# Performance work log

Hardware: AMD Instinct MI355X
Metric: run time of the kernel (lower is better)

The kernel has to match this reference:

```python
import jax, jax.numpy as jnp
import numpy as np

B, S, D = 4, 2048, 1024
H = 16
HD = D // H

def setup_inputs() -> dict:
    key = jax.random.key(0)
    ks = jax.random.split(key, 6)
    std = 1.0 / np.sqrt(D)
    x = jax.random.normal(ks[0], (B, S, D), dtype=jnp.float32)
    Wq = jax.random.uniform(ks[1], (D, D), jnp.float32, -std, std)
    Wk = jax.random.uniform(ks[2], (D, D), jnp.float32, -std, std)
    Wv = jax.random.uniform(ks[3], (D, D), jnp.float32, -std, std)
    Wo = jax.random.uniform(ks[4], (D, D), jnp.float32, -std, std)
    bo = jax.random.uniform(ks[5], (D,), jnp.float32, -std, std)
    return {"x": x, "Wq": Wq, "Wk": Wk, "Wv": Wv, "Wo": Wo, "bo": bo}

def reference(x, Wq, Wk, Wv, Wo, bo):
    b, s, _ = x.shape
    # projections; torch Linear computes x @ W^T, here W stored as (d_in, d_out)... we use (D, D) applied as x @ W
    q = (x @ Wq).reshape(b, s, H, HD).transpose(0, 2, 1, 3)  # b h s hd
    k = (x @ Wk).reshape(b, s, H, HD).transpose(0, 2, 1, 3)
    v = (x @ Wv).reshape(b, s, H, HD).transpose(0, 2, 1, 3)
    scores = jnp.einsum('bhqd,bhkd->bhqk', q, k)
    causal = jnp.triu(jnp.ones((s, s), dtype=bool), k=1)
    scores = jnp.where(causal[None, None], -jnp.inf, scores)
    attn = jax.nn.softmax(scores / np.sqrt(HD), axis=-1)  # dropout=0.0 -> identity
    ctx = jnp.einsum('bhqk,bhkd->bhqd', attn, v)
    ctx = ctx.transpose(0, 2, 1, 3).reshape(b, s, D)
    return ctx @ Wo + bo
```

## Files before the change

kernel.cpp:

```cpp
#include <hip/hip_runtime.h>

typedef unsigned short u16;
typedef __bf16 bf16x8 __attribute__((ext_vector_type(8)));
typedef float f32x4 __attribute__((ext_vector_type(4)));

#define Bn 4
#define Sn 2048
#define Dn 1024
#define Hn 16
#define HDn 64

__device__ inline u16 f2bf(float f) {
  unsigned u = __builtin_bit_cast(unsigned, f);
  u += 0x7fffu + ((u >> 16) & 1u);
  return (u16)(u >> 16);
}

__device__ __forceinline__ void gl2lds16(const u16* g, u16* l) {
  __builtin_amdgcn_global_load_lds(
      (const __attribute__((address_space(1))) unsigned int*)g,
      (__attribute__((address_space(3))) unsigned int*)l, 16, 0, 0);
}

__device__ __forceinline__ float fexp2(float x) {
  return __builtin_amdgcn_exp2f(x);
}

__device__ __forceinline__ unsigned pk_bf_trunc(float lo, float hi) {
  return __builtin_amdgcn_perm(__builtin_bit_cast(unsigned, hi),
                               __builtin_bit_cast(unsigned, lo), 0x07060302u);
}

__global__ __launch_bounds__(256) void cvt4(const float* __restrict__ in,
                                            u16* __restrict__ out, int n4) {
  int i = blockIdx.x * 256 + threadIdx.x;
  if (i < n4) {
    float4 v = ((const float4*)in)[i];
    ushort4 o;
    o.x = f2bf(v.x); o.y = f2bf(v.y); o.z = f2bf(v.z); o.w = f2bf(v.w);
    ((ushort4*)out)[i] = o;
  }
}

__global__ __launch_bounds__(256) void tcvt4(const float* __restrict__ w0,
                                             const float* __restrict__ w1,
                                             const float* __restrict__ w2,
                                             const float* __restrict__ w3,
                                             u16* __restrict__ out) {
  __shared__ u16 tile[32][33];
  const float* in = (blockIdx.z == 0) ? w0 : (blockIdx.z == 1) ? w1
                   : (blockIdx.z == 2) ? w2 : w3;
  u16* dst = out + (size_t)blockIdx.z * Dn * Dn;
  int bx = blockIdx.x * 32;
  int by = blockIdx.y * 32;
  int tx = threadIdx.x & 31;
  int ty = threadIdx.x >> 5;
#pragma unroll
  for (int r = 0; r < 32; r += 8)
    tile[ty + r][tx] = f2bf(in[(size_t)(by + ty + r) * Dn + bx + tx]);
  __syncthreads();
#pragma unroll
  for (int r = 0; r < 32; r += 8)
    dst[(size_t)(bx + ty + r) * Dn + by + tx] = tile[tx][ty + r];
}

__global__ __launch_bounds__(512, 2) void gemm_qkv(const u16* __restrict__ A,
                                                   const u16* __restrict__ Bt,
                                                   u16* __restrict__ qkb,
                                                   u16* __restrict__ vt,
                                                   float qscale) {
  __shared__ __attribute__((aligned(16))) u16 S[2][4][8192];

  const int tid = threadIdx.x;
  const int lane = tid & 63;
  const int lcol = lane & 15;
  const int quad = lane >> 4;
  const int wave = tid >> 6;
  const int wr = wave >> 2;
  const int wc = wave & 3;

  const int bid = blockIdx.x;
  const int swz = (bid & 7) * 48 + (bid >> 3);
  const int bm = (swz & 31) * 256;
  const int bn = (swz >> 5) * 256;

  const u16* srcp[4][2];
#pragma unroll
  for (int rg = 0; rg < 4; rg++) {
#pragma unroll
    for (int j = 0; j < 2; j++) {
      int o = j * 8192 + tid * 16;
      int l = o ^ (((o >> 8) & 7) << 4);
      int rho = l >> 7;
      int c2 = (l >> 1) & 63;
      int gr;
      if (rg == 0)      gr = bm + (rho & 63) + ((rho >> 6) << 7);
      else if (rg == 1) gr = bm + 64 + (rho & 63) + ((rho >> 6) << 7);
      else if (rg == 2) gr = bn + ((rho >> 5) << 6) + (rho & 31);
      else              gr = bn + ((rho >> 5) << 6) + 32 + (rho & 31);
      const u16* base = (rg < 2) ? A : Bt;
      srcp[rg][j] = base + (size_t)gr * Dn + c2;
    }
  }

  auto stg = [&](int rg, int buf, int tile) {
    if (tile >= 16) return;
    const int k0 = tile << 6;
    u16* d = &S[buf][rg][tid * 8];
    gl2lds16(srcp[rg][0] + k0, d);
    gl2lds16(srcp[rg][1] + k0, d + 4096);
  };

  f32x4 acc[8][4];
#pragma unroll
  for (int i = 0; i < 8; i++)
#pragma unroll
    for (int j = 0; j < 4; j++) acc[i][j] = (f32x4){0.f, 0.f, 0.f, 0.f};

  const int SW = (lcol & 14) << 3;
  const int cs0 = (quad * 16) ^ SW;
  const int cs1 = (64 + quad * 16) ^ SW;

#define PHASE(BUF, QR, QC, STG_STMT, WAIT_STMT)                               \
  {                                                                           \
    const char* Ab = (const char*)&S[BUF][QR][0];                             \
    const char* Bb = (const char*)&S[BUF][2 + QC][0];                         \
    bf16x8 af0[4], af1[4], bf0[2], bf1[2];                                    \
    _Pragma("unroll") for (int mi = 0; mi < 4; mi++) {                        \
      int r = (wr * 64 + mi * 16 + lcol) * 128;                               \
      af0[mi] = *(const bf16x8*)(Ab + (r + cs0));                             \
      af1[mi] = *(const bf16x8*)(Ab + (r + cs1));                             \
    }                                                                         \
    _Pragma("unroll") for (int ni = 0; ni < 2; ni++) {                        \
      int r = (wc * 32 + ni * 16 + lcol) * 128;                               \
      bf0[ni] = *(const bf16x8*)(Bb + (r + cs0));                             \
      bf1[ni] = *(const bf16x8*)(Bb + (r + cs1));                             \
    }                                                                         \
    STG_STMT;                                                                 \
    WAIT_STMT;                                                                \
    __builtin_amdgcn_s_barrier();                                             \
    asm volatile("s_waitcnt lgkmcnt(0)" ::: "memory");                        \
    __builtin_amdgcn_sched_barrier(0);                                        \
    __builtin_amdgcn_s_setprio(1);                                            \
    _Pragma("unroll") for (int mi = 0; mi < 4; mi++)                          \
      _Pragma("unroll") for (int ni = 0; ni < 2; ni++) {                      \
        acc[QR * 4 + mi][QC * 2 + ni] =                                       \
            __builtin_amdgcn_mfma_f32_16x16x32_bf16(                          \
                af0[mi], bf0[ni], acc[QR * 4 + mi][QC * 2 + ni], 0, 0, 0);    \
        acc[QR * 4 + mi][QC * 2 + ni] =                                       \
            __builtin_amdgcn_mfma_f32_16x16x32_bf16(                          \
                af1[mi], bf1[ni], acc[QR * 4 + mi][QC * 2 + ni], 0, 0, 0);    \
      }                                                                       \
    __builtin_amdgcn_s_setprio(0);                                            \
    __builtin_amdgcn_s_barrier();                                             \
  }

  stg(0, 0, 0); stg(2, 0, 0); stg(1, 0, 0); stg(3, 0, 0);
  stg(0, 1, 1); stg(2, 1, 1);
  asm volatile("s_waitcnt vmcnt(4)" ::: "memory");
  __builtin_amdgcn_s_barrier();

#pragma unroll 1
  for (int I = 0; I < 8; ++I) {
    const int t1 = 2 * I + 1, t2 = 2 * I + 2, t3 = 2 * I + 3;
    PHASE(0, 0, 0, stg(1, 1, t1), );
    PHASE(0, 0, 1, stg(3, 1, t1), );
    PHASE(0, 1, 0, stg(0, 0, t2), );
    PHASE(0, 1, 1, stg(2, 0, t2),
          if (I < 7) asm volatile("s_waitcnt vmcnt(4)" ::: "memory");
          else asm volatile("s_waitcnt vmcnt(0)" ::: "memory"));
    PHASE(1, 0, 0, stg(1, 0, t2), );
    PHASE(1, 0, 1, stg(3, 0, t2), );
    PHASE(1, 1, 0, stg(0, 1, t3), );
    PHASE(1, 1, 1, stg(2, 1, t3),
          if (I < 7) asm volatile("s_waitcnt vmcnt(4)" ::: "memory"));
  }
#undef PHASE

  const int rb = bm + wr * 128 + quad * 4;
  const int cb = bn + wc * 64 + lcol;
  if (bn >= 2048) {
#pragma unroll
    for (int ai = 0; ai < 8; ai++) {
#pragma unroll
      for (int bj = 0; bj < 4; bj++) {
        int row0 = rb + ((ai >> 2) << 6) + ((ai & 3) << 4);
        int s = row0 & (Sn - 1);
        int bb = row0 >> 11;
        int vcol = cb + ((bj >> 1) << 5) + ((bj & 1) << 4) - 2048;
        int bh = (bb << 4) + (vcol >> 6);
        int hd = vcol & 63;
        unsigned d0 = (unsigned)f2bf(acc[ai][bj][0]) |
                      ((unsigned)f2bf(acc[ai][bj][1]) << 16);
        unsigned d1 = (unsigned)f2bf(acc[ai][bj][2]) |
                      ((unsigned)f2bf(acc[ai][bj][3]) << 16);
        *(uint2*)(vt + ((size_t)bh * HDn + hd) * Sn + s) = (uint2){d0, d1};
      }
    }
  } else {
    const float scale = (bn < 1024) ? qscale : 1.0f;
#pragma unroll
    for (int ai = 0; ai < 8; ai++) {
#pragma unroll
      for (int bj = 0; bj < 4; bj++) {
        int row0 = rb + ((ai >> 2) << 6) + ((ai & 3) << 4);
        int col = cb + ((bj >> 1) << 5) + ((bj & 1) << 4);
#pragma unroll
        for (int r = 0; r < 4; r++)
          qkb[(size_t)(row0 + r) * 2048 + col] = f2bf(acc[ai][bj][r] * scale);
      }
    }
  }
}

__global__ __launch_bounds__(256) void gemm_out(const u16* __restrict__ A,
                                                const u16* __restrict__ Bt,
                                                float* __restrict__ Cout,
                                                const float* __restrict__ bias) {
  __shared__ __attribute__((aligned(16))) u16 As[2][2][128][32];
  __shared__ __attribute__((aligned(16))) u16 Bs[2][2][128][32];
  const int K = Dn;
  const int t = threadIdx.x;
  const int wave = t >> 6;
  const int lane = t & 63;
  const int lcol = lane & 15;
  const int quad = lane >> 4;
  const int wm = (wave >> 1) * 64;
  const int wn = (wave & 1) * 64;
  const int bm = blockIdx.y * 128;
  const int bn = blockIdx.x * 128;

  const int srow = lane >> 2;
  const int sseg = (lane & 3) * 8;
  const u16* a0p = A + (size_t)(bm + wave * 16 + srow) * K + sseg;
  const u16* a1p = a0p + (size_t)64 * K;
  const u16* b0p = Bt + (size_t)(bn + wave * 16 + srow) * K + sseg;
  const u16* b1p = b0p + (size_t)64 * K;
  u16* asl = &As[0][0][0][0] + wave * 512 + lane * 8;
  u16* bsl = &Bs[0][0][0][0] + wave * 512 + lane * 8;

  auto stage = [&](int k0, int d) {
    u16* as = asl + d * 8192;
    u16* bs = bsl + d * 8192;
    gl2lds16(a0p + k0, as);
    gl2lds16(a1p + k0, as + 2048);
    gl2lds16(a0p + k0 + 32, as + 4096);
    gl2lds16(a1p + k0 + 32, as + 6144);
    gl2lds16(b0p + k0, bs);
    gl2lds16(b1p + k0, bs + 2048);
    gl2lds16(b0p + k0 + 32, bs + 4096);
    gl2lds16(b1p + k0 + 32, bs + 6144);
  };

  f32x4 acc[4][4];
#pragma unroll
  for (int i = 0; i < 4; i++)
#pragma unroll
    for (int j = 0; j < 4; j++) acc[i][j] = (f32x4){0.f, 0.f, 0.f, 0.f};

  stage(0, 0);
  int d = 0;
  for (int k0 = 0; k0 < K; k0 += 64, d ^= 1) {
    __syncthreads();
    if (k0 + 64 < K) stage(k0 + 64, d ^ 1);
#pragma unroll
    for (int ks = 0; ks < 2; ks++) {
      bf16x8 af[4], bf[4];
#pragma unroll
      for (int mi = 0; mi < 4; mi++)
        af[mi] = *(const bf16x8*)(&As[d][ks][wm + mi * 16 + lcol][quad * 8]);
#pragma unroll
      for (int ni = 0; ni < 4; ni++)
        bf[ni] = *(const bf16x8*)(&Bs[d][ks][wn + ni * 16 + lcol][quad * 8]);
#pragma unroll
      for (int mi = 0; mi < 4; mi++)
#pragma unroll
        for (int ni = 0; ni < 4; ni++)
          acc[mi][ni] = __builtin_amdgcn_mfma_f32_16x16x32_bf16(af[mi], bf[ni], acc[mi][ni], 0, 0, 0);
    }
  }

#pragma unroll
  for (int mi = 0; mi < 4; mi++) {
#pragma unroll
    for (int ni = 0; ni < 4; ni++) {
#pragma unroll
      for (int r = 0; r < 4; r++) {
        int row = bm + wm + mi * 16 + quad * 4 + r;
        int col = bn + wn + ni * 16 + lcol;
        Cout[(size_t)row * Dn + col] = acc[mi][ni][r] + bias[col];
      }
    }
  }
}

__global__ __launch_bounds__(256, 2) void attn5(const u16* __restrict__ QK,
                                                const u16* __restrict__ Vt,
                                                u16* __restrict__ ctx) {
  __shared__ __attribute__((aligned(16))) u16 Ks2[2][64][32];
  __shared__ __attribute__((aligned(16))) u16 Vts2[2][64][32];
  __shared__ __attribute__((aligned(16))) u16 Pt[4][32][72];

  const int bh = blockIdx.x;
  const int b = bh >> 4, h = bh & 15;
  const int pair = blockIdx.y;
  const int t = threadIdx.x;
  const int w = t >> 6;
  const int lane = t & 63;
  const int lcol = lane & 15;
  const int quad = lane >> 4;
  const int qw0 = pair * 128 + w * 32;
  const int qw1 = (15 - pair) * 128 + w * 32;

  const size_t qkbase = ((size_t)b * Sn) * 2048 + h * HDn;
  const size_t obase = ((size_t)b * Sn) * Dn + h * HDn;
  const size_t vbase = ((size_t)bh * HDn) * Sn;

  bf16x8 qf[2][2][2];
#pragma unroll
  for (int si = 0; si < 2; si++) {
    const int qws = si ? qw1 : qw0;
#pragma unroll
    for (int qb = 0; qb < 2; qb++) {
      const u16* qp = QK + qkbase + (size_t)(qws + qb * 16 + lcol) * 2048 + quad * 8;
      qf[si][qb][0] = *(const bf16x8*)qp;
      qf[si][qb][1] = *(const bf16x8*)(qp + 32);
    }
  }

  f32x4 o[2][2][4];
#pragma unroll
  for (int si = 0; si < 2; si++)
#pragma unroll
    for (int qb = 0; qb < 2; qb++)
#pragma unroll
      for (int nb = 0; nb < 4; nb++) o[si][qb][nb] = (f32x4){0.f, 0.f, 0.f, 0.f};
  float lsum[2][2] = {{0.f, 0.f}, {0.f, 0.f}};

  const int srow = lane >> 2;
  const int sseg = (lane & 3) * 8;
  const u16* kp0 = QK + qkbase + 1024 + (size_t)(w * 16 + srow) * 2048 + sseg;
  const u16* vp0 = Vt + vbase + (size_t)(w * 16 + srow) * Sn + sseg;
  u16* ksl0 = &Ks2[0][0][0] + w * 512 + lane * 8;
  u16* ksl1 = ksl0 + 2048;
  u16* vsl0 = &Vts2[0][0][0] + w * 512 + lane * 8;
  u16* vsl1 = vsl0 + 2048;

  auto do_strip = [&](int si, int qw, int j0) {
    f32x4 s[4][2];
#pragma unroll
    for (int mb = 0; mb < 4; mb++) {
      bf16x8 kf0 = *(const bf16x8*)(&Ks2[0][mb * 16 + lcol][quad * 8]);
      bf16x8 kf1 = *(const bf16x8*)(&Ks2[1][mb * 16 + lcol][quad * 8]);
#pragma unroll
      for (int qb = 0; qb < 2; qb++) {
        f32x4 a = (f32x4){0.f, 0.f, 0.f, 0.f};
        a = __builtin_amdgcn_mfma_f32_16x16x32_bf16(kf0, qf[si][qb][0], a, 0, 0, 0);
        a = __builtin_amdgcn_mfma_f32_16x16x32_bf16(kf1, qf[si][qb][1], a, 0, 0, 0);
        s[mb][qb] = a;
      }
    }

    const bool needmask = (j0 + 63 > qw);
#pragma unroll
    for (int qb = 0; qb < 2; qb++) {
      const int qrow = qw + qb * 16 + lcol;
#pragma unroll
      for (int mb = 0; mb < 4; mb++) {
        float p[4];
#pragma unroll
        for (int r = 0; r < 4; r++) p[r] = fexp2(s[mb][qb][r]);
        if (needmask) {
          const int kvb = j0 + mb * 16 + quad * 4;
#pragma unroll
          for (int r = 0; r < 4; r++)
            if (kvb + r > qrow) p[r] = 0.f;
        }
        lsum[si][qb] += (p[0] + p[1]) + (p[2] + p[3]);
        unsigned d0 = pk_bf_trunc(p[0], p[1]);
        unsigned d1 = pk_bf_trunc(p[2], p[3]);
        *(uint2*)(&Pt[w][qb * 16 + lcol][mb * 16 + quad * 4]) = (uint2){d0, d1};
      }
    }

#pragma unroll
    for (int c = 0; c < 2; c++) {
      bf16x8 pf0 = *(const bf16x8*)(&Pt[w][lcol][c * 32 + quad * 8]);
      bf16x8 pf1 = *(const bf16x8*)(&Pt[w][16 + lcol][c * 32 + quad * 8]);
#pragma unroll
      for (int nb = 0; nb < 4; nb++) {
        bf16x8 vf = *(const bf16x8*)(&Vts2[c][nb * 16 + lcol][quad * 8]);
        o[si][0][nb] = __builtin_amdgcn_mfma_f32_16x16x32_bf16(vf, pf0, o[si][0][nb], 0, 0, 0);
        o[si][1][nb] = __builtin_amdgcn_mfma_f32_16x16x32_bf16(vf, pf1, o[si][1][nb], 0, 0, 0);
      }
    }
  };

  const int n_kv = (15 - pair) * 128 + 128;

  for (int j0 = 0; j0 < n_kv; j0 += 64) {
    {
      const u16* kp = kp0 + (size_t)j0 * 2048;
      gl2lds16(kp, ksl0);
      gl2lds16(kp + 32, ksl1);
      const u16* vp = vp0 + j0;
      gl2lds16(vp, vsl0);
      gl2lds16(vp + 32, vsl1);
    }
    __syncthreads();

    if (j0 <= qw1 + 31) do_strip(1, qw1, j0);
    if (j0 <= qw0 + 31) do_strip(0, qw0, j0);
    __syncthreads();
  }

#pragma unroll
  for (int si = 0; si < 2; si++) {
    const int qws = si ? qw1 : qw0;
#pragma unroll
    for (int qb = 0; qb < 2; qb++) {
      float l = lsum[si][qb];
      l += __shfl_xor(l, 16);
      l += __shfl_xor(l, 32);
      float inv = 1.0f / l;
#pragma unroll
      for (int nb = 0; nb < 4; nb++) {
        unsigned d0 = (unsigned)f2bf(o[si][qb][nb][0] * inv) |
                      ((unsigned)f2bf(o[si][qb][nb][1] * inv) << 16);
        unsigned d1 = (unsigned)f2bf(o[si][qb][nb][2] * inv) |
                      ((unsigned)f2bf(o[si][qb][nb][3] * inv) << 16);
        u16* p = ctx + obase + (size_t)(qws + qb * 16 + lcol) * Dn + nb * 16 + quad * 4;
        *(uint2*)p = (uint2){d0, d1};
      }
    }
  }
}

extern "C" void kernel_launch(void* const* d_in, const int* in_sizes, int n_in,
                              void* d_out, int out_size, void* d_ws, size_t ws_size,
                              hipStream_t stream) {
  const float* x  = (const float*)d_in[0];
  const float* Wq = (const float*)d_in[1];
  const float* Wk = (const float*)d_in[2];
  const float* Wv = (const float*)d_in[3];
  const float* Wo = (const float*)d_in[4];
  const float* bo = (const float*)d_in[5];
  float* out = (float*)d_out;

  const size_t BSD = (size_t)Bn * Sn * Dn;
  const size_t DD = (size_t)Dn * Dn;

  u16* xb    = (u16*)d_ws;
  u16* wall  = xb + BSD;
  u16* qkb   = wall + 4 * DD;
  u16* vt    = qkb + 2 * BSD;
  u16* cb    = vt + BSD;

  cvt4<<<(int)(BSD / 4 / 256), 256, 0, stream>>>(x, xb, (int)(BSD / 4));
  tcvt4<<<dim3(Dn / 32, Dn / 32, 4), 256, 0, stream>>>(Wq, Wk, Wv, Wo, wall);

  gemm_qkv<<<dim3(384), 512, 0, stream>>>(xb, wall, qkb, vt,
                                          0.125f * 1.44269504f);

  attn5<<<dim3(Bn * Hn, 8), 256, 0, stream>>>(qkb, vt, cb);

  gemm_out<<<dim3(Dn / 128, (Bn * Sn) / 128), 256, 0, stream>>>(cb, wall + 3 * DD, out, bo);
}
```

Baseline: 253.3 us.

## Restructure QKV GEMM main loop to cache B fragments and reorder staging

```diff
diff --git a/kernel.cpp b/kernel.cpp
--- a/kernel.cpp
+++ b/kernel.cpp
@@ -80,9 +80,8 @@
   const int wc = wave & 3;
 
   const int bid = blockIdx.x;
-  const int swz = (bid & 7) * 48 + (bid >> 3);
-  const int bm = (swz & 31) * 256;
-  const int bn = (swz >> 5) * 256;
+  const int bm = ((bid & 7) * 4 + ((bid >> 3) & 3)) * 256;
+  const int bn = (bid >> 5) * 256;
 
   const u16* srcp[4][2];
 #pragma unroll
@@ -121,61 +120,67 @@
   const int cs0 = (quad * 16) ^ SW;
   const int cs1 = (64 + quad * 16) ^ SW;
 
-#define PHASE(BUF, QR, QC, STG_STMT, WAIT_STMT)                               \
-  {                                                                           \
-    const char* Ab = (const char*)&S[BUF][QR][0];                             \
-    const char* Bb = (const char*)&S[BUF][2 + QC][0];                         \
-    bf16x8 af0[4], af1[4], bf0[2], bf1[2];                                    \
-    _Pragma("unroll") for (int mi = 0; mi < 4; mi++) {                        \
-      int r = (wr * 64 + mi * 16 + lcol) * 128;                               \
-      af0[mi] = *(const bf16x8*)(Ab + (r + cs0));                             \
-      af1[mi] = *(const bf16x8*)(Ab + (r + cs1));                             \
-    }                                                                         \
-    _Pragma("unroll") for (int ni = 0; ni < 2; ni++) {                        \
-      int r = (wc * 32 + ni * 16 + lcol) * 128;                               \
-      bf0[ni] = *(const bf16x8*)(Bb + (r + cs0));                             \
-      bf1[ni] = *(const bf16x8*)(Bb + (r + cs1));                             \
-    }                                                                         \
-    STG_STMT;                                                                 \
-    WAIT_STMT;                                                                \
-    __builtin_amdgcn_s_barrier();                                             \
-    asm volatile("s_waitcnt lgkmcnt(0)" ::: "memory");                        \
-    __builtin_amdgcn_sched_barrier(0);                                        \
-    __builtin_amdgcn_s_setprio(1);                                            \
-    _Pragma("unroll") for (int mi = 0; mi < 4; mi++)                          \
-      _Pragma("unroll") for (int ni = 0; ni < 2; ni++) {                      \
-        acc[QR * 4 + mi][QC * 2 + ni] =                                       \
-            __builtin_amdgcn_mfma_f32_16x16x32_bf16(                          \
-                af0[mi], bf0[ni], acc[QR * 4 + mi][QC * 2 + ni], 0, 0, 0);    \
-        acc[QR * 4 + mi][QC * 2 + ni] =                                       \
-            __builtin_amdgcn_mfma_f32_16x16x32_bf16(                          \
-                af1[mi], bf1[ni], acc[QR * 4 + mi][QC * 2 + ni], 0, 0, 0);    \
-      }                                                                       \
-    __builtin_amdgcn_s_setprio(0);                                            \
-    __builtin_amdgcn_s_barrier();                                             \
-  }
-
-  stg(0, 0, 0); stg(2, 0, 0); stg(1, 0, 0); stg(3, 0, 0);
-  stg(0, 1, 1); stg(2, 1, 1);
-  asm volatile("s_waitcnt vmcnt(4)" ::: "memory");
+  bf16x8 bk0[4], bk1[4];
+
+#define MFMA16(a, b, c) __builtin_amdgcn_mfma_f32_16x16x32_bf16(a, b, c, 0, 0, 0)
+
+#define ARD(D, Q, F, K)                                                      \
+  (*(const bf16x8*)((const char*)&S[D][(Q) >> 1][0] +                        \
+      ((wr * 64 + ((Q) & 1) * 32 + (F) * 16 + lcol) * 128 +                  \
+       ((K) ? cs1 : cs0))))
+#define BRD(D, NI, K)                                                        \
+  (*(const bf16x8*)((const char*)&S[D][2 + ((NI) >> 1)][0] +                 \
+      ((wc * 32 + ((NI) & 1) * 16 + lcol) * 128 + ((K) ? cs1 : cs0))))
+
+#define PHASE(D, T, Q, DO_B, STG_RG, WAIT)                                   \
+  {                                                                          \
+    bf16x8 a00 = ARD(D, Q, 0, 0), a01 = ARD(D, Q, 0, 1);                     \
+    bf16x8 a10 = ARD(D, Q, 1, 0), a11 = ARD(D, Q, 1, 1);                     \
+    if (DO_B) {                                                              \
+      _Pragma("unroll") for (int ni = 0; ni < 4; ni++) {                     \
+        bk0[ni] = BRD(D, ni, 0);                                             \
+        bk1[ni] = BRD(D, ni, 1);                                             \
+      }                                                                      \
+    }                                                                        \
+    stg(STG_RG, (D) ^ 1, (T) + 1);                                           \
+    WAIT;                                                                    \
+    __builtin_amdgcn_s_barrier();                                            \
+    asm volatile("s_waitcnt lgkmcnt(0)" ::: "memory");                       \
+    __builtin_amdgcn_sched_barrier(0);                                       \
+    __builtin_amdgcn_s_setprio(1);                                           \
+    _Pragma("unroll") for (int ni = 0; ni < 4; ni++) {                       \
+      acc[(Q) * 2][ni] = MFMA16(a00, bk0[ni], acc[(Q) * 2][ni]);             \
+      acc[(Q) * 2][ni] = MFMA16(a01, bk1[ni], acc[(Q) * 2][ni]);             \
+      acc[(Q) * 2 + 1][ni] = MFMA16(a10, bk0[ni], acc[(Q) * 2 + 1][ni]);     \
+      acc[(Q) * 2 + 1][ni] = MFMA16(a11, bk1[ni], acc[(Q) * 2 + 1][ni]);     \
+    }                                                                        \
+    __builtin_amdgcn_s_setprio(0);                                           \
+    __builtin_amdgcn_s_barrier();                                            \
+  }
+
+#define TILE(D, T)                                                           \
+  PHASE(D, T, 0, 1, 2, )                                                     \
+  PHASE(D, T, 1, 0, 3,                                                       \
+        if ((T) < 15) asm volatile("s_waitcnt vmcnt(4)" ::: "memory");       \
+        else asm volatile("s_waitcnt vmcnt(0)" ::: "memory"))                \
+  PHASE(D, T, 2, 0, 0, )                                                     \
+  PHASE(D, T, 3, 0, 1, asm volatile("s_waitcnt vmcnt(2)" ::: "memory"))
+
+  stg(2, 0, 0); stg(3, 0, 0); stg(0, 0, 0); stg(1, 0, 0);
+  asm volatile("s_waitcnt vmcnt(2)" ::: "memory");
   __builtin_amdgcn_s_barrier();
 
 #pragma unroll 1
   for (int I = 0; I < 8; ++I) {
-    const int t1 = 2 * I + 1, t2 = 2 * I + 2, t3 = 2 * I + 3;
-    PHASE(0, 0, 0, stg(1, 1, t1), );
-    PHASE(0, 0, 1, stg(3, 1, t1), );
-    PHASE(0, 1, 0, stg(0, 0, t2), );
-    PHASE(0, 1, 1, stg(2, 0, t2),
-          if (I < 7) asm volatile("s_waitcnt vmcnt(4)" ::: "memory");
-          else asm volatile("s_waitcnt vmcnt(0)" ::: "memory"));
-    PHASE(1, 0, 0, stg(1, 0, t2), );
-    PHASE(1, 0, 1, stg(3, 0, t2), );
-    PHASE(1, 1, 0, stg(0, 1, t3), );
-    PHASE(1, 1, 1, stg(2, 1, t3),
-          if (I < 7) asm volatile("s_waitcnt vmcnt(4)" ::: "memory"));
-  }
+    const int T0 = 2 * I, T1 = 2 * I + 1;
+    TILE(0, T0)
+    TILE(1, T1)
+  }
+#undef TILE
 #undef PHASE
+#undef ARD
+#undef BRD
+#undef MFMA16
 
   const int rb = bm + wr * 128 + quad * 4;
   const int cb = bn + wc * 64 + lcol;
```

After: 241.4 us. -4.7%, faster.
